# Kernel tuning notes

Measured on AMD Instinct MI355X. Metric: run time of the kernel, lower is better.

Reference implementation:

```python
import jax, jax.numpy as jnp
import numpy as np

KH, KW = 3, 3
STRIDE, PAD, DIL = 1, 1, 1
DG = 1  # deformable groups


def setup_inputs() -> dict:
    key = jax.random.key(0)
    k1, k2, k3, k4 = jax.random.split(key, 4)
    B, C, H, W, O = 4, 64, 128, 128, 64
    x = jax.random.normal(k1, (B, C, H, W), jnp.float32)
    weight = jax.random.normal(k2, (O, C, KH, KW), jnp.float32) * 0.05
    bias = jnp.zeros((O,), jnp.float32)
    # offset/mask conv params (zero-init in original; small random here so
    # the bilinear sampling path is actually exercised)
    om_weight = jax.random.normal(k3, (DG * 3 * KH * KW, C, KH, KW), jnp.float32) * 0.01
    om_bias = jax.random.normal(k4, (DG * 3 * KH * KW,), jnp.float32) * 0.01
    return {"x": x, "weight": weight, "bias": bias,
            "om_weight": om_weight, "om_bias": om_bias}


def _dcn(x, weight, bias, om_weight, om_bias):
    B, C, H, W = x.shape
    O = weight.shape[0]
    K = KH * KW
    Cg = C // DG

    # --- offset/mask conv (plain conv2d) ---
    om = jax.lax.conv_general_dilated(
        x, om_weight, (STRIDE, STRIDE), [(PAD, PAD), (PAD, PAD)],
        dimension_numbers=("NCHW", "OIHW", "NCHW"))
    om = om + om_bias[None, :, None, None]
    Ho, Wo = om.shape[2], om.shape[3]
    o1, o2, m = jnp.split(om, 3, axis=1)            # each (B, DG*K, Ho, Wo)
    off_y = o1.reshape(B, DG, K, Ho, Wo)
    off_x = o2.reshape(B, DG, K, Ho, Wo)
    mask = jax.nn.sigmoid(m).reshape(B, DG, K, Ho, Wo)

    # --- fractional sampling positions per kernel tap ---
    ky = jnp.repeat(jnp.arange(KH), KW).astype(jnp.float32)   # (K,)
    kx = jnp.tile(jnp.arange(KW), KH).astype(jnp.float32)
    base_y = (jnp.arange(Ho, dtype=jnp.float32) * STRIDE - PAD)
    base_x = (jnp.arange(Wo, dtype=jnp.float32) * STRIDE - PAD)
    py = off_y + base_y[None, None, None, :, None] + (ky * DIL)[None, None, :, None, None]
    px = off_x + base_x[None, None, None, None, :] + (kx * DIL)[None, None, :, None, None]

    y0 = jnp.floor(py)
    x0 = jnp.floor(px)
    ly = py - y0
    lx = px - x0
    y0i = y0.astype(jnp.int32)
    x0i = x0.astype(jnp.int32)

    xg = x.reshape(B, DG, Cg, H * W)
    # gather spatial samples per (batch, group), broadcast over channels
    gather = jax.vmap(jax.vmap(lambda feat, idx: jnp.take(feat, idx, axis=-1)))

    def corner(yc, xc, w):
        valid = (yc >= 0) & (yc < H) & (xc >= 0) & (xc < W)
        idx = jnp.clip(yc, 0, H - 1) * W + jnp.clip(xc, 0, W - 1)  # (B,DG,K,Ho,Wo)
        v = gather(xg, idx.reshape(B, DG, -1)).reshape(B, DG, Cg, K, Ho, Wo)
        w = jnp.where(valid, w, 0.0)
        return v * w[:, :, None]  # zero-padded bilinear corner

    val = (corner(y0i,     x0i,     (1 - ly) * (1 - lx))
         + corner(y0i,     x0i + 1, (1 - ly) * lx)
         + corner(y0i + 1, x0i,     ly * (1 - lx))
         + corner(y0i + 1, x0i + 1, ly * lx))
    val = val * mask[:, :, None]                    # (B,DG,Cg,K,Ho,Wo)

    w4 = weight.reshape(O, DG, Cg, K)
    out = jnp.einsum("ogck,bgckhw->bohw", w4, val) + bias[None, :, None, None]
    return out


def reference(x, weight, bias, om_weight, om_bias):
    return _dcn(x, weight, bias, om_weight, om_bias)
```

## Files before the change

kernel.cpp:

```cpp
#include <hip/hip_runtime.h>
#include <hip/hip_bf16.h>
#include <math.h>

#define BB 4
#define CC 64
#define HH 128
#define WW 128
#define OO 64
#define HWW (HH * WW)

typedef short bf8 __attribute__((ext_vector_type(8)));
typedef float f32x4 __attribute__((ext_vector_type(4)));

#define WHF_OFF  0
#define WLF_OFF  73728
#define WOMH_OFF 147456
#define WOML_OFF 184320

__device__ inline unsigned short f2bf(float f) {
    union { float f; unsigned u; } x; x.f = f;
    unsigned u = x.u;
    return (unsigned short)((u + 0x7FFFu + ((u >> 16) & 1u)) >> 16);
}
__device__ inline float bf2f(unsigned short h) {
    union { unsigned u; float f; } x; x.u = ((unsigned)h) << 16;
    return x.f;
}
__device__ inline unsigned pack_rne2(float a, float b) {
    __hip_bfloat162 h2 = __float22bfloat162_rn(make_float2(a, b));
    union { __hip_bfloat162 h; unsigned u; } cv; cv.h = h2;
    return cv.u;
}

__global__ void prep_kernel(const float* __restrict__ weight,
                            const float* __restrict__ om_weight,
                            unsigned short* __restrict__ whf,
                            unsigned short* __restrict__ wlf,
                            unsigned short* __restrict__ womh,
                            unsigned short* __restrict__ woml)
{
    int d = blockIdx.x * 256 + threadIdx.x;
    if (d < 18 * 4 * 64 * 8) {
        int j  = d & 7;
        int l  = (d >> 3) & 63;
        int wv = (d >> 9) & 3;
        int ch = d >> 11;
        int o  = wv * 16 + (l & 15);
        int kk = (l >> 4) * 8 + j;
        int c  = (ch / 9) * 32 + kk;
        int tap = ch % 9;
        float w = weight[(o * CC + c) * 9 + tap];
        unsigned short h = f2bf(w);
        whf[d] = h;
        wlf[d] = f2bf(w - bf2f(h));
    }
    int d2 = d - 18 * 4 * 64 * 8;
    if (d2 >= 0 && d2 < 18 * 2 * 64 * 8) {
        int j  = d2 & 7;
        int l  = (d2 >> 3) & 63;
        int og = (d2 >> 9) & 1;
        int ch = d2 >> 10;
        int o  = og * 16 + (l & 15);
        int kk = (l >> 4) * 8 + j;
        int c  = (ch / 9) * 32 + kk;
        int tap = ch % 9;
        float w = (o < 27) ? om_weight[(o * CC + c) * 9 + tap] : 0.f;
        unsigned short h = f2bf(w);
        womh[d2] = h;
        woml[d2] = f2bf(w - bf2f(h));
    }
}

__global__ void __launch_bounds__(256, 4)
fused_kernel(const float* __restrict__ x,
             const unsigned short* __restrict__ whf,
             const unsigned short* __restrict__ wlf,
             const unsigned short* __restrict__ womh,
             const unsigned short* __restrict__ woml,
             const float* __restrict__ bias,
             const float* __restrict__ om_bias,
             float* __restrict__ out)
{
    __shared__ __align__(16) float Xs2[8 * 180 * 4];
    __shared__ __align__(16) unsigned vhf[2][32][21];
    __shared__ float swt[4][288];
    __shared__ int   sidx[288];

    int t    = threadIdx.x;
    int lane = t & 63;
    int wv   = t >> 6;

    int bid = blockIdx.x;
    int b   = bid >> 9;
    int r   = bid & 511;
    int ho  = r >> 2;
    int w0  = (r & 3) << 5;

    auto stage = [&](int half) {
        const float* xh = x + ((size_t)(b * CC + half * 32)) * HWW;
#pragma unroll 1
        for (int i = t; i < 1440; i += 256) {
            int cg  = i / 180;
            int pos = i - cg * 180;
            int rr  = pos / 36;
            int cc2 = pos - rr * 36;
            int gy = ho - 2 + rr, gx = w0 - 2 + cc2;
            bool ok = (gy >= 0) & (gy < HH) & (gx >= 0) & (gx < WW);
            int gi = ok ? gy * WW + gx : 0;
            const float* xc = xh + (size_t)cg * 4 * HWW + gi;
            float4 v;
            v.x = xc[0]; v.y = xc[HWW]; v.z = xc[2 * HWW]; v.w = xc[3 * HWW];
            if (!ok) { v.x = 0.f; v.y = 0.f; v.z = 0.f; v.w = 0.f; }
            *(float4*)&Xs2[(cg * 180 + pos) * 4] = v;
        }
    };

    f32x4 accom = (f32x4){0.f, 0.f, 0.f, 0.f};
    auto om_pass = [&](int half) {
        int og = wv & 1;
        int s  = wv >> 1;
        int pix_s = s * 16 + (lane & 15);
        int cg0   = (lane >> 4) * 2;
#pragma unroll 1
        for (int tap = 0; tap < 9; tap++) {
            int ch = half * 9 + tap;
            int ky = tap / 3, kx = tap - ky * 3;
            int pos = (ky + 1) * 36 + pix_s + kx + 1;
            float4 f0 = *(const float4*)&Xs2[(cg0 * 180 + pos) * 4];
            float4 f1 = *(const float4*)&Xs2[((cg0 + 1) * 180 + pos) * 4];
            bf8 bh;
            ((unsigned*)&bh)[0] = pack_rne2(f0.x, f0.y);
            ((unsigned*)&bh)[1] = pack_rne2(f0.z, f0.w);
            ((unsigned*)&bh)[2] = pack_rne2(f1.x, f1.y);
            ((unsigned*)&bh)[3] = pack_rne2(f1.z, f1.w);
            const bf8 ah = *(const bf8*)&womh[((size_t)(ch * 2 + og) * 64 + lane) * 8];
            const bf8 al = *(const bf8*)&woml[((size_t)(ch * 2 + og) * 64 + lane) * 8];
            accom = __builtin_amdgcn_mfma_f32_16x16x32_bf16(ah, bh, accom, 0, 0, 0);
            accom = __builtin_amdgcn_mfma_f32_16x16x32_bf16(al, bh, accom, 0, 0, 0);
        }
    };

    f32x4 acc[2];
    acc[0] = (f32x4){0.f, 0.f, 0.f, 0.f};
    acc[1] = (f32x4){0.f, 0.f, 0.f, 0.f};

    auto main_pass = [&](int half) {
        int pix = t & 31;
        int cg  = t >> 5;
        const float* xg = x + ((size_t)(b * CC + half * 32 + cg * 4)) * HWW;
#pragma unroll 1
        for (int tap = 0; tap < 9; tap++) {
            int ach  = half * 9 + tap;
            int buf  = tap & 1;
            int item = tap * 32 + pix;
            float w00 = swt[0][item], w01 = swt[1][item];
            float w10 = swt[2][item], w11 = swt[3][item];
            int sv = sidx[item];
            int y0 = ((sv >> 16) & 0x7FFF) - 16;
            int x0 = (sv & 0xFFFF) - 16;
            const bf8 ah = *(const bf8*)&whf[((size_t)(ach * 4 + wv) * 64 + lane) * 8];
            const bf8 al = *(const bf8*)&wlf[((size_t)(ach * 4 + wv) * 64 + lane) * 8];

            float v0, v1, v2, v3;
            if (sv >= 0) {
                int o00 = (y0 - ho + 2) * 36 + (x0 - w0 + 2);
                const float* Xp = &Xs2[(cg * 180 + o00) * 4];
                float4 c00 = *(const float4*)(Xp);
                float4 c01 = *(const float4*)(Xp + 4);
                float4 c10 = *(const float4*)(Xp + 144);
                float4 c11 = *(const float4*)(Xp + 148);
                v0 = w00 * c00.x + w01 * c01.x + w10 * c10.x + w11 * c11.x;
                v1 = w00 * c00.y + w01 * c01.y + w10 * c10.y + w11 * c11.y;
                v2 = w00 * c00.z + w01 * c01.z + w10 * c10.z + w11 * c11.z;
                v3 = w00 * c00.w + w01 * c01.w + w10 * c10.w + w11 * c11.w;
            } else {
                int cy0 = min(max(y0, 0), HH - 1), cy1 = min(max(y0 + 1, 0), HH - 1);
                int cx0 = min(max(x0, 0), WW - 1), cx1 = min(max(x0 + 1, 0), WW - 1);
                int i00 = cy0 * WW + cx0, i01 = cy0 * WW + cx1;
                int i10 = cy1 * WW + cx0, i11 = cy1 * WW + cx1;
                const float* x0p = xg;
                const float* x1p = xg + HWW;
                const float* x2p = xg + 2 * HWW;
                const float* x3p = xg + 3 * HWW;
                v0 = w00 * x0p[i00] + w01 * x0p[i01] + w10 * x0p[i10] + w11 * x0p[i11];
                v1 = w00 * x1p[i00] + w01 * x1p[i01] + w10 * x1p[i10] + w11 * x1p[i11];
                v2 = w00 * x2p[i00] + w01 * x2p[i01] + w10 * x2p[i10] + w11 * x2p[i11];
                v3 = w00 * x3p[i00] + w01 * x3p[i01] + w10 * x3p[i10] + w11 * x3p[i11];
            }
            uint2 hw;
            hw.x = pack_rne2(v0, v1);
            hw.y = pack_rne2(v2, v3);
            *(uint2*)&vhf[buf][pix][cg * 2] = hw;
            __syncthreads();
#pragma unroll
            for (int s2 = 0; s2 < 2; s2++) {
                const bf8 bv = *(const bf8*)&vhf[buf][s2 * 16 + (lane & 15)][(lane >> 4) * 4];
                acc[s2] = __builtin_amdgcn_mfma_f32_16x16x32_bf16(ah, bv, acc[s2], 0, 0, 0);
                acc[s2] = __builtin_amdgcn_mfma_f32_16x16x32_bf16(al, bv, acc[s2], 0, 0, 0);
            }
        }
    };

    stage(1);
    __syncthreads();
    om_pass(1);
    __syncthreads();
    stage(0);
    __syncthreads();
    om_pass(0);

    float* omL = (float*)&vhf[0][0][0];
    {
        int og = wv & 1, s = wv >> 1;
#pragma unroll
        for (int rg = 0; rg < 4; rg++) {
            int m = og * 16 + (lane >> 4) * 4 + rg;
            if (m < 27) {
                int pp = s * 16 + (lane & 15);
                float v = accom[rg] + om_bias[m];
                if (m >= 18) v = 1.f / (1.f + expf(-v));
                omL[m * 32 + pp] = v;
            }
        }
    }
    __syncthreads();

#pragma unroll 1
    for (int it = t; it < 288; it += 256) {
        int k  = it >> 5;
        int pp = it & 31;
        float oy = omL[k * 32 + pp];
        float ox = omL[(9 + k) * 32 + pp];
        float mm = omL[(18 + k) * 32 + pp];
        int ky = k / 3, kx = k - ky * 3;
        float py = oy + (float)(ho + ky - 1);
        float px = ox + (float)(w0 + pp + kx - 1);
        float fy = floorf(py), fx = floorf(px);
        float ly = py - fy, lx = px - fx;
        int y0 = (int)fy, x0 = (int)fx;
        bool vy0 = (y0 >= 0) & (y0 < HH);
        bool vy1 = (y0 + 1 >= 0) & (y0 + 1 < HH);
        bool vx0 = (x0 >= 0) & (x0 < WW);
        bool vx1 = (x0 + 1 >= 0) & (x0 + 1 < WW);
        swt[0][it] = (vy0 & vx0) ? (1.f - ly) * (1.f - lx) * mm : 0.f;
        swt[1][it] = (vy0 & vx1) ? (1.f - ly) * lx * mm : 0.f;
        swt[2][it] = (vy1 & vx0) ? ly * (1.f - lx) * mm : 0.f;
        swt[3][it] = (vy1 & vx1) ? ly * lx * mm : 0.f;
        bool inw = (y0 >= ho - 2) & (y0 <= ho + 1) & (x0 >= w0 - 2) & (x0 <= w0 + 32);
        int y0c = min(max(y0, -8), 135);
        int x0c = min(max(x0, -8), 135);
        sidx[it] = ((y0c + 16) << 16) | ((x0c + 16) & 0xFFFF)
                 | (inw ? 0 : (int)0x80000000);
    }
    __syncthreads();

    main_pass(0);
    stage(1);
    __syncthreads();
    main_pass(1);

    int prow = ho * WW + w0;
#pragma unroll
    for (int s = 0; s < 2; s++) {
#pragma unroll
        for (int rg = 0; rg < 4; rg++) {
            int o  = wv * 16 + (lane >> 4) * 4 + rg;
            int pp = s * 16 + (lane & 15);
            out[((size_t)(b * OO + o)) * HWW + prow + pp] = acc[s][rg] + bias[o];
        }
    }
}

extern "C" void kernel_launch(void* const* d_in, const int* in_sizes, int n_in,
                              void* d_out, int out_size, void* d_ws, size_t ws_size,
                              hipStream_t stream)
{
    (void)in_sizes; (void)n_in; (void)out_size; (void)ws_size;
    const float* x      = (const float*)d_in[0];
    const float* weight = (const float*)d_in[1];
    const float* bias   = (const float*)d_in[2];
    const float* om_w   = (const float*)d_in[3];
    const float* om_b   = (const float*)d_in[4];
    float* out = (float*)d_out;
    char*  ws  = (char*)d_ws;

    unsigned short* whf  = (unsigned short*)(ws + WHF_OFF);
    unsigned short* wlf  = (unsigned short*)(ws + WLF_OFF);
    unsigned short* womh = (unsigned short*)(ws + WOMH_OFF);
    unsigned short* woml = (unsigned short*)(ws + WOML_OFF);

    int prep_n = 18 * 4 * 64 * 8 + 18 * 2 * 64 * 8;
    prep_kernel<<<(prep_n + 255) / 256, 256, 0, stream>>>(weight, om_w, whf, wlf, womh, woml);

    int nblk = BB * HH * (WW / 32);
    fused_kernel<<<nblk, 256, 0, stream>>>(x, whf, wlf, womh, woml, bias, om_b, out);
}
```

Baseline: 127.3 us.

## Switch to fp16 MFMA, stage all channels once in fp16 LDS, use packed half2 bilinear

Converts the weight hi/lo split and the MFMA operands from bf16 to fp16. The input tile for all 64 channels is now staged once into shared memory as packed fp16 instead of two fp32 half-stages, which removes the restaging between passes. Bilinear interpolation in the in-window path uses packed half2 FMAs with fp16 corner weights. This shrinks shared-memory footprint and traffic and halves the interpolation ALU work, at the cost of reduced precision from fp16 accumulation of the interpolated values and fp16-quantized corner weights.

```diff
diff --git a/kernel.cpp b/kernel.cpp
--- a/kernel.cpp
+++ b/kernel.cpp
@@ -1,5 +1,5 @@
 #include <hip/hip_runtime.h>
-#include <hip/hip_bf16.h>
+#include <hip/hip_fp16.h>
 #include <math.h>
 
 #define BB 4
@@ -9,7 +9,7 @@
 #define OO 64
 #define HWW (HH * WW)
 
-typedef short bf8 __attribute__((ext_vector_type(8)));
+typedef _Float16 f16x8 __attribute__((ext_vector_type(8)));
 typedef float f32x4 __attribute__((ext_vector_type(4)));
 
 #define WHF_OFF  0
@@ -17,19 +17,11 @@
 #define WOMH_OFF 147456
 #define WOML_OFF 184320
 
-__device__ inline unsigned short f2bf(float f) {
-    union { float f; unsigned u; } x; x.f = f;
-    unsigned u = x.u;
-    return (unsigned short)((u + 0x7FFFu + ((u >> 16) & 1u)) >> 16);
-}
-__device__ inline float bf2f(unsigned short h) {
-    union { unsigned u; float f; } x; x.u = ((unsigned)h) << 16;
-    return x.f;
-}
-__device__ inline unsigned pack_rne2(float a, float b) {
-    __hip_bfloat162 h2 = __float22bfloat162_rn(make_float2(a, b));
-    union { __hip_bfloat162 h; unsigned u; } cv; cv.h = h2;
-    return cv.u;
+__device__ inline __half2 u2h(unsigned u) {
+    union { unsigned u; __half2 h; } c; c.u = u; return c.h;
+}
+__device__ inline unsigned h2u(__half2 h) {
+    union { __half2 h; unsigned u; } c; c.h = h; return c.u;
 }
 
 __global__ void prep_kernel(const float* __restrict__ weight,
@@ -50,9 +42,10 @@
         int c  = (ch / 9) * 32 + kk;
         int tap = ch % 9;
         float w = weight[(o * CC + c) * 9 + tap];
-        unsigned short h = f2bf(w);
-        whf[d] = h;
-        wlf[d] = f2bf(w - bf2f(h));
+        __half h = __float2half_rn(w);
+        __half lo = __float2half_rn(w - __half2float(h));
+        whf[d] = __half_as_ushort(h);
+        wlf[d] = __half_as_ushort(lo);
     }
     int d2 = d - 18 * 4 * 64 * 8;
     if (d2 >= 0 && d2 < 18 * 2 * 64 * 8) {
@@ -65,9 +58,10 @@
         int c  = (ch / 9) * 32 + kk;
         int tap = ch % 9;
         float w = (o < 27) ? om_weight[(o * CC + c) * 9 + tap] : 0.f;
-        unsigned short h = f2bf(w);
-        womh[d2] = h;
-        woml[d2] = f2bf(w - bf2f(h));
+        __half h = __float2half_rn(w);
+        __half lo = __float2half_rn(w - __half2float(h));
+        womh[d2] = __half_as_ushort(h);
+        woml[d2] = __half_as_ushort(lo);
     }
 }
 
@@ -81,10 +75,10 @@
              const float* __restrict__ om_bias,
              float* __restrict__ out)
 {
-    __shared__ __align__(16) float Xs2[8 * 180 * 4];
+    __shared__ __align__(16) uint2 Xf[16 * 180];
     __shared__ __align__(16) unsigned vhf[2][32][21];
-    __shared__ float swt[4][288];
-    __shared__ int   sidx[288];
+    __shared__ __align__(16) uint4 swth4[288];
+    __shared__ int sidx[288];
 
     int t    = threadIdx.x;
     int lane = t & 63;
@@ -96,10 +90,10 @@
     int ho  = r >> 2;
     int w0  = (r & 3) << 5;
 
-    auto stage = [&](int half) {
-        const float* xh = x + ((size_t)(b * CC + half * 32)) * HWW;
-#pragma unroll 1
-        for (int i = t; i < 1440; i += 256) {
+    {
+        const float* xb = x + (size_t)b * CC * HWW;
+#pragma unroll 1
+        for (int i = t; i < 16 * 180; i += 256) {
             int cg  = i / 180;
             int pos = i - cg * 180;
             int rr  = pos / 36;
@@ -107,107 +101,39 @@
             int gy = ho - 2 + rr, gx = w0 - 2 + cc2;
             bool ok = (gy >= 0) & (gy < HH) & (gx >= 0) & (gx < WW);
             int gi = ok ? gy * WW + gx : 0;
-            const float* xc = xh + (size_t)cg * 4 * HWW + gi;
-            float4 v;
-            v.x = xc[0]; v.y = xc[HWW]; v.z = xc[2 * HWW]; v.w = xc[3 * HWW];
-            if (!ok) { v.x = 0.f; v.y = 0.f; v.z = 0.f; v.w = 0.f; }
-            *(float4*)&Xs2[(cg * 180 + pos) * 4] = v;
-        }
-    };
+            const float* xc = xb + (size_t)cg * 4 * HWW + gi;
+            float v0 = xc[0], v1 = xc[HWW], v2 = xc[2 * HWW], v3 = xc[3 * HWW];
+            if (!ok) { v0 = 0.f; v1 = 0.f; v2 = 0.f; v3 = 0.f; }
+            uint2 p;
+            p.x = h2u(__floats2half2_rn(v0, v1));
+            p.y = h2u(__floats2half2_rn(v2, v3));
+            Xf[cg * 180 + pos] = p;
+        }
+    }
+    __syncthreads();
 
     f32x4 accom = (f32x4){0.f, 0.f, 0.f, 0.f};
-    auto om_pass = [&](int half) {
+    {
         int og = wv & 1;
         int s  = wv >> 1;
         int pix_s = s * 16 + (lane & 15);
-        int cg0   = (lane >> 4) * 2;
-#pragma unroll 1
-        for (int tap = 0; tap < 9; tap++) {
-            int ch = half * 9 + tap;
+#pragma unroll 1
+        for (int ch = 0; ch < 18; ch++) {
+            int half = ch / 9;
+            int tap  = ch - half * 9;
+            int cg0  = half * 8 + (lane >> 4) * 2;
             int ky = tap / 3, kx = tap - ky * 3;
             int pos = (ky + 1) * 36 + pix_s + kx + 1;
-            float4 f0 = *(const float4*)&Xs2[(cg0 * 180 + pos) * 4];
-            float4 f1 = *(const float4*)&Xs2[((cg0 + 1) * 180 + pos) * 4];
-            bf8 bh;
-            ((unsigned*)&bh)[0] = pack_rne2(f0.x, f0.y);
-            ((unsigned*)&bh)[1] = pack_rne2(f0.z, f0.w);
-            ((unsigned*)&bh)[2] = pack_rne2(f1.x, f1.y);
-            ((unsigned*)&bh)[3] = pack_rne2(f1.z, f1.w);
-            const bf8 ah = *(const bf8*)&womh[((size_t)(ch * 2 + og) * 64 + lane) * 8];
-            const bf8 al = *(const bf8*)&woml[((size_t)(ch * 2 + og) * 64 + lane) * 8];
-            accom = __builtin_amdgcn_mfma_f32_16x16x32_bf16(ah, bh, accom, 0, 0, 0);
-            accom = __builtin_amdgcn_mfma_f32_16x16x32_bf16(al, bh, accom, 0, 0, 0);
-        }
-    };
-
-    f32x4 acc[2];
-    acc[0] = (f32x4){0.f, 0.f, 0.f, 0.f};
-    acc[1] = (f32x4){0.f, 0.f, 0.f, 0.f};
-
-    auto main_pass = [&](int half) {
-        int pix = t & 31;
-        int cg  = t >> 5;
-        const float* xg = x + ((size_t)(b * CC + half * 32 + cg * 4)) * HWW;
-#pragma unroll 1
-        for (int tap = 0; tap < 9; tap++) {
-            int ach  = half * 9 + tap;
-            int buf  = tap & 1;
-            int item = tap * 32 + pix;
-            float w00 = swt[0][item], w01 = swt[1][item];
-            float w10 = swt[2][item], w11 = swt[3][item];
-            int sv = sidx[item];
-            int y0 = ((sv >> 16) & 0x7FFF) - 16;
-            int x0 = (sv & 0xFFFF) - 16;
-            const bf8 ah = *(const bf8*)&whf[((size_t)(ach * 4 + wv) * 64 + lane) * 8];
-            const bf8 al = *(const bf8*)&wlf[((size_t)(ach * 4 + wv) * 64 + lane) * 8];
-
-            float v0, v1, v2, v3;
-            if (sv >= 0) {
-                int o00 = (y0 - ho + 2) * 36 + (x0 - w0 + 2);
-                const float* Xp = &Xs2[(cg * 180 + o00) * 4];
-                float4 c00 = *(const float4*)(Xp);
-                float4 c01 = *(const float4*)(Xp + 4);
-                float4 c10 = *(const float4*)(Xp + 144);
-                float4 c11 = *(const float4*)(Xp + 148);
-                v0 = w00 * c00.x + w01 * c01.x + w10 * c10.x + w11 * c11.x;
-                v1 = w00 * c00.y + w01 * c01.y + w10 * c10.y + w11 * c11.y;
-                v2 = w00 * c00.z + w01 * c01.z + w10 * c10.z + w11 * c11.z;
-                v3 = w00 * c00.w + w01 * c01.w + w10 * c10.w + w11 * c11.w;
-            } else {
-                int cy0 = min(max(y0, 0), HH - 1), cy1 = min(max(y0 + 1, 0), HH - 1);
-                int cx0 = min(max(x0, 0), WW - 1), cx1 = min(max(x0 + 1, 0), WW - 1);
-                int i00 = cy0 * WW + cx0, i01 = cy0 * WW + cx1;
-                int i10 = cy1 * WW + cx0, i11 = cy1 * WW + cx1;
-                const float* x0p = xg;
-                const float* x1p = xg + HWW;
-                const float* x2p = xg + 2 * HWW;
-                const float* x3p = xg + 3 * HWW;
-                v0 = w00 * x0p[i00] + w01 * x0p[i01] + w10 * x0p[i10] + w11 * x0p[i11];
-                v1 = w00 * x1p[i00] + w01 * x1p[i01] + w10 * x1p[i10] + w11 * x1p[i11];
-                v2 = w00 * x2p[i00] + w01 * x2p[i01] + w10 * x2p[i10] + w11 * x2p[i11];
-                v3 = w00 * x3p[i00] + w01 * x3p[i01] + w10 * x3p[i10] + w11 * x3p[i11];
-            }
-            uint2 hw;
-            hw.x = pack_rne2(v0, v1);
-            hw.y = pack_rne2(v2, v3);
-            *(uint2*)&vhf[buf][pix][cg * 2] = hw;
-            __syncthreads();
-#pragma unroll
-            for (int s2 = 0; s2 < 2; s2++) {
-                const bf8 bv = *(const bf8*)&vhf[buf][s2 * 16 + (lane & 15)][(lane >> 4) * 4];
-                acc[s2] = __builtin_amdgcn_mfma_f32_16x16x32_bf16(ah, bv, acc[s2], 0, 0, 0);
-                acc[s2] = __builtin_amdgcn_mfma_f32_16x16x32_bf16(al, bv, acc[s2], 0, 0, 0);
-            }
-        }
-    };
-
-    stage(1);
-    __syncthreads();
-    om_pass(1);
-    __syncthreads();
-    stage(0);
-    __syncthreads();
-    om_pass(0);
+            uint2 pa = Xf[cg0 * 180 + pos];
+            uint2 pb = Xf[(cg0 + 1) * 180 + pos];
+            union { f16x8 v; unsigned u[4]; } B;
+            B.u[0] = pa.x; B.u[1] = pa.y; B.u[2] = pb.x; B.u[3] = pb.y;
+            const f16x8 ah = *(const f16x8*)&womh[((size_t)(ch * 2 + og) * 64 + lane) * 8];
+            const f16x8 al = *(const f16x8*)&woml[((size_t)(ch * 2 + og) * 64 + lane) * 8];
+            accom = __builtin_amdgcn_mfma_f32_16x16x32_f16(ah, B.v, accom, 0, 0, 0);
+            accom = __builtin_amdgcn_mfma_f32_16x16x32_f16(al, B.v, accom, 0, 0, 0);
+        }
+    }
 
     float* omL = (float*)&vhf[0][0][0];
     {
@@ -242,10 +168,16 @@
         bool vy1 = (y0 + 1 >= 0) & (y0 + 1 < HH);
         bool vx0 = (x0 >= 0) & (x0 < WW);
         bool vx1 = (x0 + 1 >= 0) & (x0 + 1 < WW);
-        swt[0][it] = (vy0 & vx0) ? (1.f - ly) * (1.f - lx) * mm : 0.f;
-        swt[1][it] = (vy0 & vx1) ? (1.f - ly) * lx * mm : 0.f;
-        swt[2][it] = (vy1 & vx0) ? ly * (1.f - lx) * mm : 0.f;
-        swt[3][it] = (vy1 & vx1) ? ly * lx * mm : 0.f;
+        float w00 = (vy0 & vx0) ? (1.f - ly) * (1.f - lx) * mm : 0.f;
+        float w01 = (vy0 & vx1) ? (1.f - ly) * lx * mm : 0.f;
+        float w10 = (vy1 & vx0) ? ly * (1.f - lx) * mm : 0.f;
+        float w11 = (vy1 & vx1) ? ly * lx * mm : 0.f;
+        uint4 wp;
+        wp.x = h2u(__float2half2_rn(w00));
+        wp.y = h2u(__float2half2_rn(w01));
+        wp.z = h2u(__float2half2_rn(w10));
+        wp.w = h2u(__float2half2_rn(w11));
+        swth4[it] = wp;
         bool inw = (y0 >= ho - 2) & (y0 <= ho + 1) & (x0 >= w0 - 2) & (x0 <= w0 + 32);
         int y0c = min(max(y0, -8), 135);
         int x0c = min(max(x0, -8), 135);
@@ -254,10 +186,77 @@
     }
     __syncthreads();
 
-    main_pass(0);
-    stage(1);
-    __syncthreads();
-    main_pass(1);
+    f32x4 acc[2];
+    acc[0] = (f32x4){0.f, 0.f, 0.f, 0.f};
+    acc[1] = (f32x4){0.f, 0.f, 0.f, 0.f};
+
+    {
+        int pix = t & 31;
+        int cg  = t >> 5;
+#pragma unroll 1
+        for (int ach = 0; ach < 18; ach++) {
+            int half = ach / 9;
+            int tap  = ach - half * 9;
+            int buf  = ach & 1;
+            int cgg  = half * 8 + cg;
+            const uint2* Xrow = &Xf[cgg * 180];
+            int item = tap * 32 + pix;
+            uint4 wp = swth4[item];
+            int sv = sidx[item];
+            int y0 = ((sv >> 16) & 0x7FFF) - 16;
+            int x0 = (sv & 0xFFFF) - 16;
+            const f16x8 ah = *(const f16x8*)&whf[((size_t)(ach * 4 + wv) * 64 + lane) * 8];
+            const f16x8 al = *(const f16x8*)&wlf[((size_t)(ach * 4 + wv) * 64 + lane) * 8];
+
+            uint2 hw;
+            if (sv >= 0) {
+                int o00 = (y0 - ho + 2) * 36 + (x0 - w0 + 2);
+                uint2 c00 = Xrow[o00];
+                uint2 c01 = Xrow[o00 + 1];
+                uint2 c10 = Xrow[o00 + 36];
+                uint2 c11 = Xrow[o00 + 37];
+                __half2 w00 = u2h(wp.x), w01 = u2h(wp.y);
+                __half2 w10 = u2h(wp.z), w11 = u2h(wp.w);
+                __half2 vA = __hmul2(w00, u2h(c00.x));
+                vA = __hfma2(w01, u2h(c01.x), vA);
+                vA = __hfma2(w10, u2h(c10.x), vA);
+                vA = __hfma2(w11, u2h(c11.x), vA);
+                __half2 vB = __hmul2(w00, u2h(c00.y));
+                vB = __hfma2(w01, u2h(c01.y), vB);
+                vB = __hfma2(w10, u2h(c10.y), vB);
+                vB = __hfma2(w11, u2h(c11.y), vB);
+                hw.x = h2u(vA);
+                hw.y = h2u(vB);
+            } else {
+                const float* xg = x + ((size_t)(b * CC + half * 32 + cg * 4)) * HWW;
+                float w00f = __low2float(u2h(wp.x)), w01f = __low2float(u2h(wp.y));
+                float w10f = __low2float(u2h(wp.z)), w11f = __low2float(u2h(wp.w));
+                int cy0 = min(max(y0, 0), HH - 1), cy1 = min(max(y0 + 1, 0), HH - 1);
+                int cx0 = min(max(x0, 0), WW - 1), cx1 = min(max(x0 + 1, 0), WW - 1);
+                int i00 = cy0 * WW + cx0, i01 = cy0 * WW + cx1;
+                int i10 = cy1 * WW + cx0, i11 = cy1 * WW + cx1;
+                float v0 = w00f * xg[i00] + w01f * xg[i01] + w10f * xg[i10] + w11f * xg[i11];
+                const float* x1p = xg + HWW;
+                float v1 = w00f * x1p[i00] + w01f * x1p[i01] + w10f * x1p[i10] + w11f * x1p[i11];
+                const float* x2p = xg + 2 * HWW;
+                float v2 = w00f * x2p[i00] + w01f * x2p[i01] + w10f * x2p[i10] + w11f * x2p[i11];
+                const float* x3p = xg + 3 * HWW;
+                float v3 = w00f * x3p[i00] + w01f * x3p[i01] + w10f * x3p[i10] + w11f * x3p[i11];
+                hw.x = h2u(__floats2half2_rn(v0, v1));
+                hw.y = h2u(__floats2half2_rn(v2, v3));
+            }
+            *(uint2*)&vhf[buf][pix][cg * 2] = hw;
+            __syncthreads();
+#pragma unroll
+            for (int s2 = 0; s2 < 2; s2++) {
+                union { f16x8 v; unsigned u[4]; } B;
+                const unsigned* src = &vhf[buf][s2 * 16 + (lane & 15)][(lane >> 4) * 4];
+                B.u[0] = src[0]; B.u[1] = src[1]; B.u[2] = src[2]; B.u[3] = src[3];
+                acc[s2] = __builtin_amdgcn_mfma_f32_16x16x32_f16(ah, B.v, acc[s2], 0, 0, 0);
+                acc[s2] = __builtin_amdgcn_mfma_f32_16x16x32_f16(al, B.v, acc[s2], 0, 0, 0);
+            }
+        }
+    }
 
     int prow = ho * WW + w0;
 #pragma unroll
```

Result: no change. 128.7 us (+1.1%).
